# Optimization experiments

Hardware: AMD Instinct MI355X
Metric: run time of the kernel (lower is better)

Reference implementation:

```python
import jax, jax.numpy as jnp
import numpy as np

B = 512
D_MODEL = 512
D_STATE = 128
D_CONV = 2
EXPAND = 2
D_INNER = EXPAND * D_MODEL          # 1024
DT_RANK = (D_MODEL + 15) // 16      # 32 (mamba default 'auto')
HIDDEN = 256


def setup_inputs() -> dict:
    key = jax.random.key(0)
    ks = jax.random.split(key, 12)
    s = 0.02
    f32 = jnp.float32
    inp = {
        "x": jax.random.normal(ks[0], (B, D_MODEL), f32),
        # Mamba params (torch Linear weight layout: [out, in])
        "in_proj_w": jax.random.normal(ks[1], (2 * D_INNER, D_MODEL), f32) * s,
        "conv_w": jax.random.normal(ks[2], (D_INNER, D_CONV), f32) * s,  # depthwise kernel
        "conv_b": jnp.zeros((D_INNER,), f32),
        "x_proj_w": jax.random.normal(ks[3], (DT_RANK + 2 * D_STATE, D_INNER), f32) * s,
        "dt_proj_w": jax.random.normal(ks[4], (D_INNER, DT_RANK), f32) * s,
        "dt_proj_b": jax.random.normal(ks[5], (D_INNER,), f32) * s,
        "A_log": jnp.log(jnp.broadcast_to(
            jnp.arange(1, D_STATE + 1, dtype=f32), (D_INNER, D_STATE)).copy()),
        "D": jnp.ones((D_INNER,), f32),
        "out_proj_w": jax.random.normal(ks[6], (D_MODEL, D_INNER), f32) * s,
        # head params
        "fc1_w": jax.random.normal(ks[7], (HIDDEN, D_MODEL), f32) * s,
        "fc1_b": jnp.zeros((HIDDEN,), f32),
        "fc5_w": jax.random.normal(ks[8], (1, HIDDEN), f32) * s,
        "fc5_b": jnp.zeros((1,), f32),
    }
    return inp


def _mamba(x3, in_proj_w, conv_w, conv_b, x_proj_w, dt_proj_w, dt_proj_b,
           A_log, D, out_proj_w):
    # x3: [B, L, d_model]
    Bn, L, _ = x3.shape
    xz = jnp.einsum('bld,ed->ble', x3, in_proj_w)          # [B, L, 2*d_inner]
    xin, z = xz[..., :D_INNER], xz[..., D_INNER:]
    # depthwise causal conv1d (kernel D_CONV, padding D_CONV-1, truncated to L)
    xp = jnp.pad(xin, ((0, 0), (D_CONV - 1, 0), (0, 0)))
    conv = conv_b
    for k in range(D_CONV):
        conv = conv + conv_w[:, k] * xp[:, k:k + L, :]
    xin = jax.nn.silu(conv)                                 # [B, L, d_inner]
    x_dbl = jnp.einsum('blc,ec->ble', xin, x_proj_w)        # [B, L, dt_rank+2*d_state]
    dt = x_dbl[..., :DT_RANK]
    Bm = x_dbl[..., DT_RANK:DT_RANK + D_STATE]              # [B, L, d_state]
    Cm = x_dbl[..., DT_RANK + D_STATE:]                     # [B, L, d_state]
    dt = jax.nn.softplus(jnp.einsum('blr,cr->blc', dt, dt_proj_w) + dt_proj_b)
    A = -jnp.exp(A_log)                                     # [d_inner, d_state]
    dA = jnp.exp(dt[..., None] * A)                         # [B, L, d_inner, d_state]
    dBu = dt[..., None] * Bm[:, :, None, :] * xin[..., None]

    def step(h, t):
        dA_t, dBu_t, C_t = t
        h = dA_t * h + dBu_t                                # [B, d_inner, d_state]
        y_t = jnp.einsum('bcs,bs->bc', h, C_t)
        return h, y_t

    h0 = jnp.zeros((Bn, D_INNER, D_STATE), x3.dtype)
    _, ys = jax.lax.scan(step, h0, (dA.transpose(1, 0, 2, 3),
                                    dBu.transpose(1, 0, 2, 3),
                                    Cm.transpose(1, 0, 2)))
    y = ys.transpose(1, 0, 2)                               # [B, L, d_inner]
    y = (y + D * xin) * jax.nn.silu(z)
    return jnp.einsum('blc,dc->bld', y, out_proj_w)         # [B, L, d_model]


def reference(x, in_proj_w, conv_w, conv_b, x_proj_w, dt_proj_w, dt_proj_b,
              A_log, D, out_proj_w, fc1_w, fc1_b, fc5_w, fc5_b):
    h = _mamba(x[:, None, :], in_proj_w, conv_w, conv_b, x_proj_w,
               dt_proj_w, dt_proj_b, A_log, D, out_proj_w)[:, 0, :]
    h = h @ fc1_w.T + fc1_b
    h = jnp.where(h >= 0, h, 0.1 * h)   # LeakyReLU(0.1); dropout is eval-mode identity
    h = h @ fc5_w.T + fc5_b
    return jax.nn.sigmoid(h)            # [B, 1]
```

## Files before the change

### kernel.cpp

```cpp
#include <hip/hip_runtime.h>
#include <hip/hip_bf16.h>
#include <cstddef>

typedef __attribute__((ext_vector_type(8))) short short8;
typedef __attribute__((ext_vector_type(4))) float f32x4;

#define MFMA16(a, b, c) __builtin_amdgcn_mfma_f32_16x16x32_bf16((a), (b), (c), 0, 0, 0)

static __device__ __forceinline__ unsigned short f2bf(float f) {
    unsigned int u = __float_as_uint(f);
    u = (u + 0x7FFFu + ((u >> 16) & 1u)) >> 16;
    return (unsigned short)u;
}
static __device__ __forceinline__ float bf2f(unsigned short h) {
    return __uint_as_float(((unsigned int)h) << 16);
}
static __device__ __forceinline__ float silu_f(float v) { return v / (1.f + expf(-v)); }

static __device__ __forceinline__ short8 cvt_frag(const float* __restrict__ p) {
    float4 a = *reinterpret_cast<const float4*>(p);
    float4 b = *reinterpret_cast<const float4*>(p + 4);
    union { short8 s; unsigned int u[4]; } r;
    asm("v_cvt_pk_bf16_f32 %0, %1, %2" : "=v"(r.u[0]) : "v"(a.x), "v"(a.y));
    asm("v_cvt_pk_bf16_f32 %0, %1, %2" : "=v"(r.u[1]) : "v"(a.z), "v"(a.w));
    asm("v_cvt_pk_bf16_f32 %0, %1, %2" : "=v"(r.u[2]) : "v"(b.x), "v"(b.y));
    asm("v_cvt_pk_bf16_f32 %0, %1, %2" : "=v"(r.u[3]) : "v"(b.z), "v"(b.w));
    return r.s;
}

enum : size_t {
    O_XIN  = 0,
    O_SZ   = O_XIN  + 512 * 1024,
    O_XDBL = O_SZ   + 512 * 1024,
    O_Y    = O_XDBL + 512 * 288,
    O_MOUT = O_Y    + 512 * 1024,
};

__global__ __launch_bounds__(256, 2) void k_s1(
    const float* __restrict__ x, const float* __restrict__ wip,
    const float* __restrict__ cw, const float* __restrict__ cb,
    unsigned short* __restrict__ wsb)
{
    const int tid = threadIdx.x;
    const int w = tid >> 6, lane = tid & 63, l15 = lane & 15, g = lane >> 4;
    const int n0 = blockIdx.x * 64;
    const int m0 = blockIdx.y * 64 + w * 16;

    const float* arow = x   + (size_t)(m0 + l15) * 512 + g * 8;
    const float* brow = wip + (size_t)(n0 + l15) * 512 + g * 8;

    f32x4 acc[4] = {};
#pragma unroll 4
    for (int k0 = 0; k0 < 512; k0 += 32) {
        short8 a = cvt_frag(arow + k0);
#pragma unroll
        for (int f = 0; f < 4; ++f) {
            short8 b = cvt_frag(brow + (size_t)f * 16 * 512 + k0);
            acc[f] = MFMA16(a, b, acc[f]);
        }
    }

    const bool xhalf = (n0 < 1024);
    unsigned short* dst = wsb + (xhalf ? O_XIN : O_SZ);
#pragma unroll
    for (int f = 0; f < 4; ++f) {
        int n = n0 + f * 16 + l15;
        int c = xhalf ? n : n - 1024;
        float cwv = 0.f, cbv = 0.f;
        if (xhalf) { cwv = cw[2 * n + 1]; cbv = cb[n]; }
#pragma unroll
        for (int i = 0; i < 4; ++i) {
            int r = m0 + g * 4 + i;
            float v = acc[f][i];
            v = xhalf ? silu_f(cbv + cwv * v) : silu_f(v);
            dst[(size_t)r * 1024 + c] = f2bf(v);
        }
    }
}

__global__ __launch_bounds__(256, 2) void k_s2(
    const float* __restrict__ wxp, unsigned short* __restrict__ wsb)
{
    const int tid = threadIdx.x;
    const int w = tid >> 6, lane = tid & 63, l15 = lane & 15, g = lane >> 4;
    const int n0 = blockIdx.x * 16;
    const int m0 = blockIdx.y * 64 + w * 16;

    const unsigned short* ab = wsb + O_XIN + (size_t)(m0 + l15) * 1024 + g * 8;
    const float* brow = wxp + (size_t)(n0 + l15) * 1024 + g * 8;

    f32x4 acc = {};
#pragma unroll 4
    for (int k0 = 0; k0 < 1024; k0 += 32) {
        short8 a = *reinterpret_cast<const short8*>(ab + k0);
        short8 b = cvt_frag(brow + k0);
        acc = MFMA16(a, b, acc);
    }
    unsigned short* xd = wsb + O_XDBL;
#pragma unroll
    for (int i = 0; i < 4; ++i)
        xd[(size_t)(m0 + g * 4 + i) * 288 + n0 + l15] = f2bf(acc[i]);
}

__global__ __launch_bounds__(256, 2) void k_s3(
    const float* __restrict__ wdt, const float* __restrict__ dtb,
    const float* __restrict__ Dv,  unsigned short* __restrict__ wsb)
{
    __shared__ float bcp[16][17];
    __shared__ float bc_s[16];
    const int tid = threadIdx.x;
    const int w = tid >> 6, lane = tid & 63, l15 = lane & 15, g = lane >> 4;
    const int n0 = blockIdx.x * 256;
    const int m0 = blockIdx.y * 16;

    const unsigned short* xd = wsb + O_XDBL;
    {
        int r = tid >> 4, p = tid & 15;
        const unsigned short* row = xd + (size_t)(m0 + r) * 288;
        float s = 0.f;
#pragma unroll
        for (int q = 0; q < 8; ++q)
            s += bf2f(row[32 + p * 8 + q]) * bf2f(row[160 + p * 8 + q]);
        bcp[r][p] = s;
    }
    short8 a = *reinterpret_cast<const short8*>(xd + (size_t)(m0 + l15) * 288 + g * 8);
    __syncthreads();
    if (tid < 16) {
        float s = 0.f;
#pragma unroll
        for (int p = 0; p < 16; ++p) s += bcp[tid][p];
        bc_s[tid] = s;
    }
    __syncthreads();

    const unsigned short* xinb = wsb + O_XIN;
    const unsigned short* szb  = wsb + O_SZ;
    unsigned short* yb = wsb + O_Y;
    const f32x4 z4 = {0.f, 0.f, 0.f, 0.f};
#pragma unroll
    for (int f = 0; f < 4; ++f) {
        int n = n0 + w * 64 + f * 16 + l15;
        short8 b = cvt_frag(wdt + (size_t)n * 32 + g * 8);
        f32x4 acc = MFMA16(a, b, z4);
        float dtbv = dtb[n], Dvv = Dv[n];
#pragma unroll
        for (int i = 0; i < 4; ++i) {
            int r = m0 + g * 4 + i;
            float dtv = acc[i] + dtbv;
            dtv = (dtv > 20.f) ? dtv : log1pf(expf(dtv));
            float yv = bf2f(xinb[(size_t)r * 1024 + n]) *
                       (dtv * bc_s[g * 4 + i] + Dvv) *
                       bf2f(szb[(size_t)r * 1024 + n]);
            yb[(size_t)r * 1024 + n] = f2bf(yv);
        }
    }
}

__global__ __launch_bounds__(256, 2) void k_s4(
    const float* __restrict__ wout, unsigned short* __restrict__ wsb)
{
    const int tid = threadIdx.x;
    const int w = tid >> 6, lane = tid & 63, l15 = lane & 15, g = lane >> 4;
    const int n0 = blockIdx.x * 64 + w * 16;
    const int m0 = blockIdx.y * 16;

    const unsigned short* ab = wsb + O_Y + (size_t)(m0 + l15) * 1024 + g * 8;
    const float* brow = wout + (size_t)(n0 + l15) * 1024 + g * 8;

    f32x4 acc = {};
#pragma unroll 4
    for (int k0 = 0; k0 < 1024; k0 += 32) {
        short8 a = *reinterpret_cast<const short8*>(ab + k0);
        short8 b = cvt_frag(brow + k0);
        acc = MFMA16(a, b, acc);
    }
    unsigned short* mo = wsb + O_MOUT;
#pragma unroll
    for (int i = 0; i < 4; ++i)
        mo[(size_t)(m0 + g * 4 + i) * 512 + n0 + l15] = f2bf(acc[i]);
}

__global__ __launch_bounds__(512, 2) void k_s5(
    const float* __restrict__ wfc1, const float* __restrict__ bfc1,
    const float* __restrict__ wfc5, const float* __restrict__ bfc5,
    unsigned short* __restrict__ wsb, float* __restrict__ out)
{
    __shared__ float red[16][8];
    const int tid = threadIdx.x;
    const int w = tid >> 6, lane = tid & 63, l15 = lane & 15, g = lane >> 4;
    const int m0 = blockIdx.x * 16;

    const unsigned short* ab = wsb + O_MOUT + (size_t)(m0 + l15) * 512 + g * 8;
    const float* brow = wfc1 + (size_t)(w * 32 + l15) * 512 + g * 8;

    f32x4 acc[2] = {};
#pragma unroll 4
    for (int k0 = 0; k0 < 512; k0 += 32) {
        short8 a = *reinterpret_cast<const short8*>(ab + k0);
#pragma unroll
        for (int f = 0; f < 2; ++f) {
            short8 b = cvt_frag(brow + (size_t)f * 16 * 512 + k0);
            acc[f] = MFMA16(a, b, acc[f]);
        }
    }
    float part[4] = {0.f, 0.f, 0.f, 0.f};
#pragma unroll
    for (int f = 0; f < 2; ++f) {
        int n = w * 32 + f * 16 + l15;
        float b1 = bfc1[n], w5 = wfc5[n];
#pragma unroll
        for (int i = 0; i < 4; ++i) {
            float v = acc[f][i] + b1;
            v = v >= 0.f ? v : 0.1f * v;
            part[i] = fmaf(v, w5, part[i]);
        }
    }
#pragma unroll
    for (int off = 1; off < 16; off <<= 1)
#pragma unroll
        for (int i = 0; i < 4; ++i) part[i] += __shfl_xor(part[i], off, 64);
    if (l15 == 0)
#pragma unroll
        for (int i = 0; i < 4; ++i) red[g * 4 + i][w] = part[i];
    __syncthreads();
    if (tid < 16) {
        float s = 0.f;
#pragma unroll
        for (int j = 0; j < 8; ++j) s += red[tid][j];
        out[m0 + tid] = 1.f / (1.f + expf(-(s + bfc5[0])));
    }
}

extern "C" void kernel_launch(void* const* d_in, const int* in_sizes, int n_in,
                              void* d_out, int out_size, void* d_ws, size_t ws_size,
                              hipStream_t stream)
{
    const float* x    = (const float*)d_in[0];
    const float* wip  = (const float*)d_in[1];
    const float* cw   = (const float*)d_in[2];
    const float* cb   = (const float*)d_in[3];
    const float* wxp  = (const float*)d_in[4];
    const float* wdt  = (const float*)d_in[5];
    const float* bdt  = (const float*)d_in[6];
    const float* Dv   = (const float*)d_in[8];
    const float* wout = (const float*)d_in[9];
    const float* wfc1 = (const float*)d_in[10];
    const float* bfc1 = (const float*)d_in[11];
    const float* wfc5 = (const float*)d_in[12];
    const float* bfc5 = (const float*)d_in[13];
    float* out = (float*)d_out;

    unsigned short* wsb = (unsigned short*)d_ws;

    k_s1<<<dim3(32, 8), 256, 0, stream>>>(x, wip, cw, cb, wsb);
    k_s2<<<dim3(18, 8), 256, 0, stream>>>(wxp, wsb);
    k_s3<<<dim3(4, 32), 256, 0, stream>>>(wdt, bdt, Dv, wsb);
    k_s4<<<dim3(8, 32), 256, 0, stream>>>(wout, wsb);
    k_s5<<<dim3(32),    512, 0, stream>>>(wfc1, bfc1, wfc5, bfc5, wsb, out);
}
```

Before: 161.8 us.

## Pre-convert weights to bf16, split-K with atomics, and shrink tiles for more blocks

Adds a conversion kernel that turns the input and all weight matrices into bf16 in the workspace and zeroes fp32 accumulation buffers. The GEMM kernels then read bf16 directly instead of converting fp32 fragments inside their inner loops. k_s2 and k_s4 now split K and combine partial sums with float atomicAdd, while k_s1 and k_s3 use smaller tiles so many more blocks launch on a small problem. This trades an extra launch, a full pass over the weights and atomic traffic for more parallelism and less per-iteration conversion work.

After: 142.2 us. 12.1% less time.

```diff
diff --git a/kernel.cpp b/kernel.cpp
--- a/kernel.cpp
+++ b/kernel.cpp
@@ -29,101 +29,131 @@
 }
 
 enum : size_t {
-    O_XIN  = 0,
-    O_SZ   = O_XIN  + 512 * 1024,
-    O_XDBL = O_SZ   + 512 * 1024,
-    O_Y    = O_XDBL + 512 * 288,
-    O_MOUT = O_Y    + 512 * 1024,
+    O_X     = 0,
+    O_WIP   = O_X    + 512 * 512,
+    O_WXP   = O_WIP  + 2048 * 512,
+    O_WDT   = O_WXP  + 288 * 1024,
+    O_WOUT  = O_WDT  + 1024 * 32,
+    O_WFC1  = O_WOUT + 512 * 1024,
+    O_XIN   = O_WFC1 + 256 * 512,
+    O_SZ    = O_XIN  + 512 * 1024,
+    O_Y     = O_SZ   + 512 * 1024,
+    O_F32   = O_Y    + 512 * 1024,
 };
-
-__global__ __launch_bounds__(256, 2) void k_s1(
-    const float* __restrict__ x, const float* __restrict__ wip,
-    const float* __restrict__ cw, const float* __restrict__ cb,
+#define N_XDBLF (512 * 288)
+#define N_MOUTF (512 * 512)
+#define N_ZERO  (N_XDBLF + N_MOUTF)
+
+static __device__ __forceinline__ void cvt_seg(const float* __restrict__ s,
+                                               unsigned short* __restrict__ d,
+                                               int n, int gt, int np)
+{
+    for (int i = gt * 4; i < n; i += np * 4) {
+        float4 v = *reinterpret_cast<const float4*>(s + i);
+        ushort4 o;
+        o.x = f2bf(v.x); o.y = f2bf(v.y); o.z = f2bf(v.z); o.w = f2bf(v.w);
+        *reinterpret_cast<ushort4*>(d + i) = o;
+    }
+}
+
+__global__ __launch_bounds__(256) void k_convert(
+    const float* __restrict__ x,    const float* __restrict__ wip,
+    const float* __restrict__ wxp,  const float* __restrict__ wdt,
+    const float* __restrict__ wout, const float* __restrict__ wfc1,
     unsigned short* __restrict__ wsb)
 {
-    const int tid = threadIdx.x;
-    const int w = tid >> 6, lane = tid & 63, l15 = lane & 15, g = lane >> 4;
-    const int n0 = blockIdx.x * 64;
-    const int m0 = blockIdx.y * 64 + w * 16;
-
-    const float* arow = x   + (size_t)(m0 + l15) * 512 + g * 8;
-    const float* brow = wip + (size_t)(n0 + l15) * 512 + g * 8;
-
-    f32x4 acc[4] = {};
+    const int gt = blockIdx.x * blockDim.x + threadIdx.x;
+    const int np = gridDim.x * blockDim.x;
+    cvt_seg(x,    wsb + O_X,    512 * 512,  gt, np);
+    cvt_seg(wip,  wsb + O_WIP,  2048 * 512, gt, np);
+    cvt_seg(wxp,  wsb + O_WXP,  288 * 1024, gt, np);
+    cvt_seg(wdt,  wsb + O_WDT,  1024 * 32,  gt, np);
+    cvt_seg(wout, wsb + O_WOUT, 512 * 1024, gt, np);
+    cvt_seg(wfc1, wsb + O_WFC1, 256 * 512,  gt, np);
+    float* z = (float*)(wsb + O_F32);
+    const float4 z4 = make_float4(0.f, 0.f, 0.f, 0.f);
+    for (int i = gt * 4; i < N_ZERO; i += np * 4)
+        *reinterpret_cast<float4*>(z + i) = z4;
+}
+
+__global__ __launch_bounds__(256, 4) void k_s1(
+    unsigned short* __restrict__ wsb,
+    const float* __restrict__ cw, const float* __restrict__ cb)
+{
+    const int tid = threadIdx.x;
+    const int w = tid >> 6, lane = tid & 63, l15 = lane & 15, g = lane >> 4;
+    const int n0 = blockIdx.x * 64 + w * 16;
+    const int m0 = blockIdx.y * 16;
+
+    const unsigned short* arow = wsb + O_X   + (size_t)(m0 + l15) * 512 + g * 8;
+    const unsigned short* brow = wsb + O_WIP + (size_t)(n0 + l15) * 512 + g * 8;
+
+    f32x4 acc = {};
 #pragma unroll 4
     for (int k0 = 0; k0 < 512; k0 += 32) {
-        short8 a = cvt_frag(arow + k0);
-#pragma unroll
-        for (int f = 0; f < 4; ++f) {
-            short8 b = cvt_frag(brow + (size_t)f * 16 * 512 + k0);
-            acc[f] = MFMA16(a, b, acc[f]);
-        }
-    }
-
-    const bool xhalf = (n0 < 1024);
+        short8 a = *reinterpret_cast<const short8*>(arow + k0);
+        short8 b = *reinterpret_cast<const short8*>(brow + k0);
+        acc = MFMA16(a, b, acc);
+    }
+    const bool xhalf = (blockIdx.x < 16);
     unsigned short* dst = wsb + (xhalf ? O_XIN : O_SZ);
-#pragma unroll
-    for (int f = 0; f < 4; ++f) {
-        int n = n0 + f * 16 + l15;
-        int c = xhalf ? n : n - 1024;
-        float cwv = 0.f, cbv = 0.f;
-        if (xhalf) { cwv = cw[2 * n + 1]; cbv = cb[n]; }
-#pragma unroll
-        for (int i = 0; i < 4; ++i) {
-            int r = m0 + g * 4 + i;
-            float v = acc[f][i];
-            v = xhalf ? silu_f(cbv + cwv * v) : silu_f(v);
-            dst[(size_t)r * 1024 + c] = f2bf(v);
-        }
-    }
-}
-
-__global__ __launch_bounds__(256, 2) void k_s2(
-    const float* __restrict__ wxp, unsigned short* __restrict__ wsb)
+    int n = n0 + l15;
+    int c = xhalf ? n : n - 1024;
+    float cwv = 0.f, cbv = 0.f;
+    if (xhalf) { cwv = cw[2 * n + 1]; cbv = cb[n]; }
+#pragma unroll
+    for (int i = 0; i < 4; ++i) {
+        float v = acc[i];
+        v = xhalf ? silu_f(cbv + cwv * v) : silu_f(v);
+        dst[(size_t)(m0 + g * 4 + i) * 1024 + c] = f2bf(v);
+    }
+}
+
+__global__ __launch_bounds__(256, 4) void k_s2(
+    unsigned short* __restrict__ wsb, float* __restrict__ xdblf)
 {
     const int tid = threadIdx.x;
     const int w = tid >> 6, lane = tid & 63, l15 = lane & 15, g = lane >> 4;
     const int n0 = blockIdx.x * 16;
     const int m0 = blockIdx.y * 64 + w * 16;
-
-    const unsigned short* ab = wsb + O_XIN + (size_t)(m0 + l15) * 1024 + g * 8;
-    const float* brow = wxp + (size_t)(n0 + l15) * 1024 + g * 8;
+    const int kq = blockIdx.z * 256;
+
+    const unsigned short* arow = wsb + O_XIN + (size_t)(m0 + l15) * 1024 + kq + g * 8;
+    const unsigned short* brow = wsb + O_WXP + (size_t)(n0 + l15) * 1024 + kq + g * 8;
 
     f32x4 acc = {};
 #pragma unroll 4
-    for (int k0 = 0; k0 < 1024; k0 += 32) {
-        short8 a = *reinterpret_cast<const short8*>(ab + k0);
-        short8 b = cvt_frag(brow + k0);
+    for (int k0 = 0; k0 < 256; k0 += 32) {
+        short8 a = *reinterpret_cast<const short8*>(arow + k0);
+        short8 b = *reinterpret_cast<const short8*>(brow + k0);
         acc = MFMA16(a, b, acc);
     }
-    unsigned short* xd = wsb + O_XDBL;
 #pragma unroll
     for (int i = 0; i < 4; ++i)
-        xd[(size_t)(m0 + g * 4 + i) * 288 + n0 + l15] = f2bf(acc[i]);
-}
-
-__global__ __launch_bounds__(256, 2) void k_s3(
-    const float* __restrict__ wdt, const float* __restrict__ dtb,
-    const float* __restrict__ Dv,  unsigned short* __restrict__ wsb)
+        atomicAdd(&xdblf[(size_t)(m0 + g * 4 + i) * 288 + n0 + l15], acc[i]);
+}
+
+__global__ __launch_bounds__(256, 4) void k_s3(
+    unsigned short* __restrict__ wsb, const float* __restrict__ xdblf,
+    const float* __restrict__ dtb, const float* __restrict__ Dv)
 {
     __shared__ float bcp[16][17];
     __shared__ float bc_s[16];
     const int tid = threadIdx.x;
     const int w = tid >> 6, lane = tid & 63, l15 = lane & 15, g = lane >> 4;
-    const int n0 = blockIdx.x * 256;
+    const int n0 = blockIdx.x * 64;
     const int m0 = blockIdx.y * 16;
 
-    const unsigned short* xd = wsb + O_XDBL;
     {
         int r = tid >> 4, p = tid & 15;
-        const unsigned short* row = xd + (size_t)(m0 + r) * 288;
+        const float* row = xdblf + (size_t)(m0 + r) * 288;
         float s = 0.f;
 #pragma unroll
         for (int q = 0; q < 8; ++q)
-            s += bf2f(row[32 + p * 8 + q]) * bf2f(row[160 + p * 8 + q]);
+            s += row[32 + p * 8 + q] * row[160 + p * 8 + q];
         bcp[r][p] = s;
     }
-    short8 a = *reinterpret_cast<const short8*>(xd + (size_t)(m0 + l15) * 288 + g * 8);
+    short8 a3 = cvt_frag(xdblf + (size_t)(m0 + l15) * 288 + g * 8);
     __syncthreads();
     if (tid < 16) {
         float s = 0.f;
@@ -137,69 +167,66 @@
     const unsigned short* szb  = wsb + O_SZ;
     unsigned short* yb = wsb + O_Y;
     const f32x4 z4 = {0.f, 0.f, 0.f, 0.f};
-#pragma unroll
-    for (int f = 0; f < 4; ++f) {
-        int n = n0 + w * 64 + f * 16 + l15;
-        short8 b = cvt_frag(wdt + (size_t)n * 32 + g * 8);
-        f32x4 acc = MFMA16(a, b, z4);
-        float dtbv = dtb[n], Dvv = Dv[n];
-#pragma unroll
-        for (int i = 0; i < 4; ++i) {
-            int r = m0 + g * 4 + i;
-            float dtv = acc[i] + dtbv;
-            dtv = (dtv > 20.f) ? dtv : log1pf(expf(dtv));
-            float yv = bf2f(xinb[(size_t)r * 1024 + n]) *
-                       (dtv * bc_s[g * 4 + i] + Dvv) *
-                       bf2f(szb[(size_t)r * 1024 + n]);
-            yb[(size_t)r * 1024 + n] = f2bf(yv);
-        }
-    }
-}
-
-__global__ __launch_bounds__(256, 2) void k_s4(
-    const float* __restrict__ wout, unsigned short* __restrict__ wsb)
+    int n = n0 + w * 16 + l15;
+    short8 b = *reinterpret_cast<const short8*>(wsb + O_WDT + (size_t)n * 32 + g * 8);
+    f32x4 acc = MFMA16(a3, b, z4);
+    float dtbv = dtb[n], Dvv = Dv[n];
+#pragma unroll
+    for (int i = 0; i < 4; ++i) {
+        int r = m0 + g * 4 + i;
+        float dtv = acc[i] + dtbv;
+        dtv = (dtv > 20.f) ? dtv : log1pf(expf(dtv));
+        float yv = bf2f(xinb[(size_t)r * 1024 + n]) *
+                   (dtv * bc_s[g * 4 + i] + Dvv) *
+                   bf2f(szb[(size_t)r * 1024 + n]);
+        yb[(size_t)r * 1024 + n] = f2bf(yv);
+    }
+}
+
+__global__ __launch_bounds__(256, 4) void k_s4(
+    unsigned short* __restrict__ wsb, float* __restrict__ moutf)
 {
     const int tid = threadIdx.x;
     const int w = tid >> 6, lane = tid & 63, l15 = lane & 15, g = lane >> 4;
     const int n0 = blockIdx.x * 64 + w * 16;
     const int m0 = blockIdx.y * 16;
-
-    const unsigned short* ab = wsb + O_Y + (size_t)(m0 + l15) * 1024 + g * 8;
-    const float* brow = wout + (size_t)(n0 + l15) * 1024 + g * 8;
+    const int kq = blockIdx.z * 512;
+
+    const unsigned short* arow = wsb + O_Y    + (size_t)(m0 + l15) * 1024 + kq + g * 8;
+    const unsigned short* brow = wsb + O_WOUT + (size_t)(n0 + l15) * 1024 + kq + g * 8;
 
     f32x4 acc = {};
 #pragma unroll 4
-    for (int k0 = 0; k0 < 1024; k0 += 32) {
-        short8 a = *reinterpret_cast<const short8*>(ab + k0);
-        short8 b = cvt_frag(brow + k0);
+    for (int k0 = 0; k0 < 512; k0 += 32) {
+        short8 a = *reinterpret_cast<const short8*>(arow + k0);
+        short8 b = *reinterpret_cast<const short8*>(brow + k0);
         acc = MFMA16(a, b, acc);
     }
-    unsigned short* mo = wsb + O_MOUT;
 #pragma unroll
     for (int i = 0; i < 4; ++i)
-        mo[(size_t)(m0 + g * 4 + i) * 512 + n0 + l15] = f2bf(acc[i]);
+        atomicAdd(&moutf[(size_t)(m0 + g * 4 + i) * 512 + n0 + l15], acc[i]);
 }
 
 __global__ __launch_bounds__(512, 2) void k_s5(
-    const float* __restrict__ wfc1, const float* __restrict__ bfc1,
-    const float* __restrict__ wfc5, const float* __restrict__ bfc5,
-    unsigned short* __restrict__ wsb, float* __restrict__ out)
+    const float* __restrict__ moutf, unsigned short* __restrict__ wsb,
+    const float* __restrict__ bfc1, const float* __restrict__ wfc5,
+    const float* __restrict__ bfc5, float* __restrict__ out)
 {
     __shared__ float red[16][8];
     const int tid = threadIdx.x;
     const int w = tid >> 6, lane = tid & 63, l15 = lane & 15, g = lane >> 4;
     const int m0 = blockIdx.x * 16;
 
-    const unsigned short* ab = wsb + O_MOUT + (size_t)(m0 + l15) * 512 + g * 8;
-    const float* brow = wfc1 + (size_t)(w * 32 + l15) * 512 + g * 8;
+    const float* arow = moutf + (size_t)(m0 + l15) * 512 + g * 8;
+    const unsigned short* brow = wsb + O_WFC1 + (size_t)(w * 32 + l15) * 512 + g * 8;
 
     f32x4 acc[2] = {};
 #pragma unroll 4
     for (int k0 = 0; k0 < 512; k0 += 32) {
-        short8 a = *reinterpret_cast<const short8*>(ab + k0);
+        short8 a = cvt_frag(arow + k0);
 #pragma unroll
         for (int f = 0; f < 2; ++f) {
-            short8 b = cvt_frag(brow + (size_t)f * 16 * 512 + k0);
+            short8 b = *reinterpret_cast<const short8*>(brow + (size_t)f * 16 * 512 + k0);
             acc[f] = MFMA16(a, b, acc[f]);
         }
     }
@@ -251,10 +278,13 @@
     float* out = (float*)d_out;
 
     unsigned short* wsb = (unsigned short*)d_ws;
-
-    k_s1<<<dim3(32, 8), 256, 0, stream>>>(x, wip, cw, cb, wsb);
-    k_s2<<<dim3(18, 8), 256, 0, stream>>>(wxp, wsb);
-    k_s3<<<dim3(4, 32), 256, 0, stream>>>(wdt, bdt, Dv, wsb);
-    k_s4<<<dim3(8, 32), 256, 0, stream>>>(wout, wsb);
-    k_s5<<<dim3(32),    512, 0, stream>>>(wfc1, bfc1, wfc5, bfc5, wsb, out);
-}
+    float* xdblf = (float*)(wsb + O_F32);
+    float* moutf = xdblf + N_XDBLF;
+
+    k_convert<<<dim3(1024),    256, 0, stream>>>(x, wip, wxp, wdt, wout, wfc1, wsb);
+    k_s1     <<<dim3(32, 32),  256, 0, stream>>>(wsb, cw, cb);
+    k_s2     <<<dim3(18, 8, 4),256, 0, stream>>>(wsb, xdblf);
+    k_s3     <<<dim3(16, 32),  256, 0, stream>>>(wsb, xdblf, bdt, Dv);
+    k_s4     <<<dim3(8, 32, 2),256, 0, stream>>>(wsb, moutf);
+    k_s5     <<<dim3(32),      512, 0, stream>>>(moutf, wsb, bfc1, wfc5, bfc5, out);
+}
```
